# Optimization experiments

Measured on AMD Instinct MI355X. Metric: run time of the kernel, lower is better.

Reference implementation:

```python
import math
import jax, jax.numpy as jnp
import numpy as np

EPS = 1e-5
KS = 8          # emb_ks == emb_hs
NH = 4          # attention heads
LOOKBACK = 5
NLAYERS = 4


def prelu(x, a):
    return jnp.where(x >= 0, x, a * x)


def ln_c(x, g, b):
    # LayerNormalization4D: stats over channel dim; note (std + eps) denominator
    mu = jnp.mean(x, 1, keepdims=True)
    var = jnp.mean((x - mu) ** 2, 1, keepdims=True)
    return (x - mu) / (jnp.sqrt(var + EPS) + EPS) * g[None, :, None, None] + b[None, :, None, None]


def ln_cf_head(x, g, b):
    # x: [H, B, E, T, F]; stats over (E, F); g, b: [H, E, F]
    mu = jnp.mean(x, (2, 4), keepdims=True)
    var = jnp.mean((x - mu) ** 2, (2, 4), keepdims=True)
    return (x - mu) / (jnp.sqrt(var + EPS) + EPS) * g[:, None, :, None, :] + b[:, None, :, None, :]


def ln_cf_proj(x, g, b):
    # x: [B, C, T, F]; stats over (C, F); g, b: [C, F]
    mu = jnp.mean(x, (1, 3), keepdims=True)
    var = jnp.mean((x - mu) ** 2, (1, 3), keepdims=True)
    return (x - mu) / (jnp.sqrt(var + EPS) + EPS) * g[None, :, None, :] + b[None, :, None, :]


def lstm(x, wih, whh, bih, bhh):
    # x: [N, T, I] -> hidden sequence [N, T, H]; PyTorch gate order i, f, g, o
    xp = jnp.einsum('nti,gi->ntg', x, wih) + bih + bhh
    H = whh.shape[1]
    N = x.shape[0]

    def step(carry, xt):
        h, c = carry
        gates = xt + h @ whh.T
        i, f, g, o = jnp.split(gates, 4, axis=-1)
        c = jax.nn.sigmoid(f) * c + jax.nn.sigmoid(i) * jnp.tanh(g)
        h = jax.nn.sigmoid(o) * jnp.tanh(c)
        return (h, c), h

    init = (jnp.zeros((N, H), x.dtype), jnp.zeros((N, H), x.dtype))
    _, hs = jax.lax.scan(step, init, jnp.swapaxes(xp, 0, 1))
    return jnp.swapaxes(hs, 0, 1)


def bilstm(x, wih, whh, bih, bhh):
    fwd = lstm(x, wih[0], whh[0], bih[0], bhh[0])
    bwd = lstm(x[:, ::-1], wih[1], whh[1], bih[1], bhh[1])[:, ::-1]
    return jnp.concatenate([fwd, bwd], -1)


def unfold1d(x):
    # non-overlapping unfold (ks == stride == KS): [N, C, L] -> [N, L//KS, C*KS]
    N, C, Lx = x.shape
    return x.reshape(N, C, Lx // KS, KS).transpose(0, 2, 1, 3).reshape(N, Lx // KS, C * KS)


def fold1d(h, w, b):
    # ConvTranspose1d with stride == kernel == KS; h: [N, Lp, D], w: [D, C, KS]
    y = jnp.einsum('nld,dck->nlck', h, w)
    N, Lp, C, K = y.shape
    return y.transpose(0, 2, 1, 3).reshape(N, C, Lp * K) + b[None, :, None]


def conv2d(x, w, b):
    y = jax.lax.conv_general_dilated(x, w, (1, 1), ((1, 1), (1, 1)),
                                     dimension_numbers=('NCHW', 'OIHW', 'NCHW'))
    return y + b[None, :, None, None]


def block(x, p):
    B, C, oT, oF = x.shape
    T = math.ceil((oT - KS) / KS) * KS + KS
    F = math.ceil((oF - KS) / KS) * KS + KS
    x = jnp.pad(x, ((0, 0), (0, 0), (0, T - oT), (0, F - oF)))
    input_ = x
    # intra (frequency) bidirectional LSTM
    z = ln_c(input_, p['intra_norm_g'], p['intra_norm_b'])
    z = z.transpose(0, 2, 1, 3).reshape(B * T, C, F)
    z = unfold1d(z)                                    # [B*T, F//KS, C*KS]
    h = bilstm(z, p['intra_wih'], p['intra_whh'], p['intra_bih'], p['intra_bhh'])
    z = fold1d(h, p['intra_lin_w'], p['intra_lin_b'])  # [B*T, C, F]
    intra = z.reshape(B, T, C, F).transpose(0, 2, 1, 3) + input_
    # inter (time) causal LSTM
    z = ln_c(intra, p['inter_norm_g'], p['inter_norm_b'])
    z = z.transpose(0, 3, 1, 2).reshape(B * F, C, T)
    z = unfold1d(z)                                    # [B*F, T//KS, C*KS]
    h = lstm(z, p['inter_wih'], p['inter_whh'], p['inter_bih'], p['inter_bhh'])
    z = fold1d(h, p['inter_lin_w'], p['inter_lin_b'])  # [B*F, C, T]
    inter = z.reshape(B, F, C, T).transpose(0, 2, 3, 1) + intra
    inter = inter[..., :oT, :oF]

    # per-head 1x1-conv QKV (batched over heads) + local causal attention
    def qkv(w, b, a, g, beta):
        y = jnp.einsum('bctf,hec->hbetf', inter, w) + b[:, None, :, None, None]
        y = prelu(y, a[:, None, None, None, None])
        return ln_cf_head(y, g, beta)

    Q = qkv(p['q_w'], p['q_b'], p['q_a'], p['q_g'], p['q_beta'])
    K = qkv(p['k_w'], p['k_b'], p['k_a'], p['k_g'], p['k_beta'])
    V = qkv(p['v_w'], p['v_b'], p['v_a'], p['v_g'], p['v_beta'])
    E = Q.shape[2]
    CV = V.shape[2]
    Qf = Q.transpose(0, 1, 3, 2, 4).reshape(NH, B, oT, E * oF)
    Kf = K.transpose(0, 1, 3, 2, 4).reshape(NH, B, oT, E * oF)
    Vf = V.transpose(0, 1, 3, 2, 4).reshape(NH, B, oT, CV * oF)
    attn = jnp.einsum('hbtd,hbsd->hbts', Qf, Kf) / jnp.sqrt(jnp.asarray(E * oF, Qf.dtype))
    t = jnp.arange(oT)
    d = t[:, None] - t[None, :]
    mask = (d >= 0) & (d <= LOOKBACK)      # causal with 5-frame lookback
    attn = jnp.where(mask, attn, -1e30)
    A = jax.nn.softmax(attn, axis=-1)
    O = jnp.einsum('hbts,hbsd->hbtd', A, Vf).reshape(NH, B, oT, CV, oF)
    O = O.transpose(1, 0, 3, 2, 4).reshape(B, NH * CV, oT, oF)
    y = jnp.einsum('bctf,dc->bdtf', O, p['proj_w']) + p['proj_b'][None, :, None, None]
    y = prelu(y, p['proj_a'])
    y = ln_cf_proj(y, p['proj_g'], p['proj_beta'])
    return y + inter


def _forward(x, conv_w, conv_b, gn_g, gn_b,
             intra_norm_g, intra_norm_b, intra_wih, intra_whh, intra_bih, intra_bhh,
             intra_lin_w, intra_lin_b,
             inter_norm_g, inter_norm_b, inter_wih, inter_whh, inter_bih, inter_bhh,
             inter_lin_w, inter_lin_b,
             q_w, q_b, q_a, q_g, q_beta,
             k_w, k_b, k_a, k_g, k_beta,
             v_w, v_b, v_a, v_g, v_beta,
             proj_w, proj_b, proj_a, proj_g, proj_beta,
             deconv_w, deconv_b):
    esti = conv2d(x, conv_w, conv_b)
    # GroupNorm(1, emb_dim): per-sample stats over (C, T, F), per-channel affine
    mu = jnp.mean(esti, (1, 2, 3), keepdims=True)
    var = jnp.mean((esti - mu) ** 2, (1, 2, 3), keepdims=True)
    esti = (esti - mu) / jnp.sqrt(var + EPS) * gn_g[None, :, None, None] + gn_b[None, :, None, None]
    stacked = dict(
        intra_norm_g=intra_norm_g, intra_norm_b=intra_norm_b,
        intra_wih=intra_wih, intra_whh=intra_whh, intra_bih=intra_bih, intra_bhh=intra_bhh,
        intra_lin_w=intra_lin_w, intra_lin_b=intra_lin_b,
        inter_norm_g=inter_norm_g, inter_norm_b=inter_norm_b,
        inter_wih=inter_wih, inter_whh=inter_whh, inter_bih=inter_bih, inter_bhh=inter_bhh,
        inter_lin_w=inter_lin_w, inter_lin_b=inter_lin_b,
        q_w=q_w, q_b=q_b, q_a=q_a, q_g=q_g, q_beta=q_beta,
        k_w=k_w, k_b=k_b, k_a=k_a, k_g=k_g, k_beta=k_beta,
        v_w=v_w, v_b=v_b, v_a=v_a, v_g=v_g, v_beta=v_beta,
        proj_w=proj_w, proj_b=proj_b, proj_a=proj_a, proj_g=proj_g, proj_beta=proj_beta,
    )
    for l in range(NLAYERS):
        p = {k: v[l] for k, v in stacked.items()}
        esti = block(esti, p)
    # ConvTranspose2d(k=3, s=1, p=1) == conv with spatially flipped, io-swapped kernel, pad 1
    w2 = jnp.flip(deconv_w, (2, 3)).transpose(1, 0, 2, 3)
    return conv2d(esti, w2, deconv_b)


def setup_inputs() -> dict:
    key = jax.random.key(0)
    keys = iter(jax.random.split(key, 80))

    def rn(shape, s=0.05):
        return jax.random.normal(next(keys), shape, jnp.float32) * s

    L, C, H, E, CV, FA = 4, 32, 256, 4, 8, 161
    IN = C * KS
    return dict(
        x=jax.random.normal(next(keys), (8, 2, 504, 161), jnp.float32),
        conv_w=rn((C, 2, 3, 3)), conv_b=jnp.zeros((C,), jnp.float32),
        gn_g=jnp.ones((C,), jnp.float32), gn_b=jnp.zeros((C,), jnp.float32),
        intra_norm_g=jnp.ones((L, C), jnp.float32), intra_norm_b=jnp.zeros((L, C), jnp.float32),
        intra_wih=rn((L, 2, 4 * H, IN)), intra_whh=rn((L, 2, 4 * H, H)),
        intra_bih=jnp.zeros((L, 2, 4 * H), jnp.float32), intra_bhh=jnp.zeros((L, 2, 4 * H), jnp.float32),
        intra_lin_w=rn((L, 2 * H, C, KS)), intra_lin_b=jnp.zeros((L, C), jnp.float32),
        inter_norm_g=jnp.ones((L, C), jnp.float32), inter_norm_b=jnp.zeros((L, C), jnp.float32),
        inter_wih=rn((L, 4 * H, IN)), inter_whh=rn((L, 4 * H, H)),
        inter_bih=jnp.zeros((L, 4 * H), jnp.float32), inter_bhh=jnp.zeros((L, 4 * H), jnp.float32),
        inter_lin_w=rn((L, H, C, KS)), inter_lin_b=jnp.zeros((L, C), jnp.float32),
        q_w=rn((L, NH, E, C)), q_b=jnp.zeros((L, NH, E), jnp.float32),
        q_a=jnp.full((L, NH), 0.25, jnp.float32),
        q_g=jnp.ones((L, NH, E, FA), jnp.float32), q_beta=jnp.zeros((L, NH, E, FA), jnp.float32),
        k_w=rn((L, NH, E, C)), k_b=jnp.zeros((L, NH, E), jnp.float32),
        k_a=jnp.full((L, NH), 0.25, jnp.float32),
        k_g=jnp.ones((L, NH, E, FA), jnp.float32), k_beta=jnp.zeros((L, NH, E, FA), jnp.float32),
        v_w=rn((L, NH, CV, C)), v_b=jnp.zeros((L, NH, CV), jnp.float32),
        v_a=jnp.full((L, NH), 0.25, jnp.float32),
        v_g=jnp.ones((L, NH, CV, FA), jnp.float32), v_beta=jnp.zeros((L, NH, CV, FA), jnp.float32),
        proj_w=rn((L, C, C)), proj_b=jnp.zeros((L, C), jnp.float32),
        proj_a=jnp.full((L,), 0.25, jnp.float32),
        proj_g=jnp.ones((L, C, FA), jnp.float32), proj_beta=jnp.zeros((L, C, FA), jnp.float32),
        deconv_w=rn((C, 2, 3, 3)), deconv_b=jnp.zeros((2,), jnp.float32),
    )


def reference(x, conv_w, conv_b, gn_g, gn_b,
              intra_norm_g, intra_norm_b, intra_wih, intra_whh, intra_bih, intra_bhh,
              intra_lin_w, intra_lin_b,
              inter_norm_g, inter_norm_b, inter_wih, inter_whh, inter_bih, inter_bhh,
              inter_lin_w, inter_lin_b,
              q_w, q_b, q_a, q_g, q_beta,
              k_w, k_b, k_a, k_g, k_beta,
              v_w, v_b, v_a, v_g, v_beta,
              proj_w, proj_b, proj_a, proj_g, proj_beta,
              deconv_w, deconv_b):
    return _forward(x, conv_w, conv_b, gn_g, gn_b,
                    intra_norm_g, intra_norm_b, intra_wih, intra_whh, intra_bih, intra_bhh,
                    intra_lin_w, intra_lin_b,
                    inter_norm_g, inter_norm_b, inter_wih, inter_whh, inter_bih, inter_bhh,
                    inter_lin_w, inter_lin_b,
                    q_w, q_b, q_a, q_g, q_beta,
                    k_w, k_b, k_a, k_g, k_beta,
                    v_w, v_b, v_a, v_g, v_beta,
                    proj_w, proj_b, proj_a, proj_g, proj_beta,
                    deconv_w, deconv_b)
```

## Files before the change

kernel.cpp:

```cpp
#include <hip/hip_runtime.h>
#include <hip/hip_bf16.h>
#include <math.h>

#define BB   8
#define CH   32
#define TT   504
#define FFp  168
#define OF   161
#define KSZ  8
#define HID  256
#define NG   1024
#define NHh  4
#define EE   4
#define CVv  8
#define N1   4032
#define N2   1344
#define LFi  21
#define LTi  63
#define EPSf 1e-5f

#define AS1 __attribute__((address_space(1)))
#define AS3 __attribute__((address_space(3)))

typedef __hip_bfloat16 bf16;
typedef __attribute__((ext_vector_type(8))) short s16x8;
typedef __attribute__((ext_vector_type(4))) float f32x4;

__device__ __forceinline__ float b2f(bf16 v) { return __bfloat162float(v); }
__device__ __forceinline__ bf16 f2b(float v) { return __float2bfloat16(v); }
__device__ __forceinline__ float us2f(unsigned short u) {
  return __uint_as_float(((unsigned)u) << 16);
}
__device__ __forceinline__ unsigned short f2bu(float v) {
  unsigned u = __float_as_uint(v);
  unsigned r = u + 0x7fffu + ((u >> 16) & 1u);
  return (unsigned short)(r >> 16);
}

__device__ __forceinline__ float sigm(float x) { return 1.f / (1.f + __expf(-x)); }
__device__ __forceinline__ float tanh_f(float x) {
  x = fminf(15.f, fmaxf(-15.f, x));
  float e = __expf(2.f * x);
  return (e - 1.f) / (e + 1.f);
}

__device__ __forceinline__ void block_reduce2(float& s1, float& s2, float* red) {
#pragma unroll
  for (int off = 32; off > 0; off >>= 1) {
    s1 += __shfl_down(s1, off, 64);
    s2 += __shfl_down(s2, off, 64);
  }
  int lane = threadIdx.x & 63, wv = threadIdx.x >> 6;
  __syncthreads();
  if (lane == 0) { red[wv * 2] = s1; red[wv * 2 + 1] = s2; }
  __syncthreads();
  s1 = red[0] + red[2] + red[4] + red[6];
  s2 = red[1] + red[3] + red[5] + red[7];
}

__global__ __launch_bounds__(192) void conv_in_k(const float* __restrict__ x,
                                                 const float* __restrict__ w,
                                                 const float* __restrict__ bias,
                                                 bf16* __restrict__ out) {
  __shared__ float xs[2 * 3 * (OF + 3)];
  int bt = blockIdx.x;
  int b = bt / TT, t = bt % TT;
  int tid = threadIdx.x;
  for (int i = tid; i < 2 * 3 * (OF + 3); i += 192) {
    int ci = i / (3 * (OF + 3));
    int rem = i % (3 * (OF + 3));
    int rr = rem / (OF + 3);
    int f = rem % (OF + 3);
    int ts = t + rr - 1;
    float v = 0.f;
    if (ts >= 0 && ts < TT && f < OF) v = x[((size_t)(b * 2 + ci) * TT + ts) * OF + f];
    xs[i] = v;
  }
  __syncthreads();
  int f = tid;
  if (f < OF) {
    float xv[2][3][3];
#pragma unroll
    for (int ci = 0; ci < 2; ci++)
#pragma unroll
      for (int kh = 0; kh < 3; kh++)
#pragma unroll
        for (int kw = 0; kw < 3; kw++) {
          int ff = f + kw - 1;
          xv[ci][kh][kw] = (ff < 0) ? 0.f : xs[(ci * 3 + kh) * (OF + 3) + ff];
        }
    for (int co = 0; co < CH; co++) {
      float acc = bias[co];
#pragma unroll
      for (int ci = 0; ci < 2; ci++)
#pragma unroll
        for (int kh = 0; kh < 3; kh++)
#pragma unroll
          for (int kw = 0; kw < 3; kw++)
            acc += xv[ci][kh][kw] * w[((co * 2 + ci) * 3 + kh) * 3 + kw];
      out[((size_t)(b * CH + co) * TT + t) * OF + f] = f2b(acc);
    }
  }
}

__global__ __launch_bounds__(256) void gn_reduce_k(const bf16* __restrict__ xin,
                                                   float* __restrict__ stats) {
  const int M = CH * TT * OF;
  int b = blockIdx.x >> 6;
  int part = blockIdx.x & 63;
  const bf16* p = xin + (size_t)b * M;
  float s1 = 0.f, s2 = 0.f;
  for (int i = part * 256 + threadIdx.x; i < M; i += 64 * 256) {
    float v = b2f(p[i]);
    s1 += v; s2 += v * v;
  }
  __shared__ float red[8];
  block_reduce2(s1, s2, red);
  if (threadIdx.x == 0) {
    atomicAdd(&stats[b * 2], s1);
    atomicAdd(&stats[b * 2 + 1], s2);
  }
}

__global__ __launch_bounds__(256) void gn_apply_k(const bf16* __restrict__ xin,
                                                  const float* __restrict__ stats,
                                                  const float* __restrict__ g,
                                                  const float* __restrict__ bb,
                                                  bf16* __restrict__ act) {
  int gid = blockIdx.x * 256 + threadIdx.x;
  int f = gid % FFp;
  int t = (gid / FFp) % TT;
  int c = (gid / (FFp * TT)) % CH;
  int b = gid / (FFp * TT * CH);
  float v = 0.f;
  if (f < OF) {
    const float M = (float)(CH * TT * OF);
    float mu = stats[b * 2] / M;
    float var = stats[b * 2 + 1] / M - mu * mu;
    float xv = b2f(xin[((size_t)(b * CH + c) * TT + t) * OF + f]);
    v = (xv - mu) * rsqrtf(var + EPSf) * g[c] + bb[c];
  }
  act[gid] = f2b(v);
}

__global__ __launch_bounds__(256) void ln_unfold_k(const bf16* __restrict__ xin,
                                                   const float* __restrict__ g,
                                                   const float* __restrict__ bb,
                                                   bf16* __restrict__ out) {
  __shared__ float sm[CH * FFp];
  __shared__ float mu_s[FFp], rs_s[FFp];
  __shared__ float gg[CH], bv[CH];
  int bt = blockIdx.x;
  int b = bt / TT, t = bt % TT;
  int tid = threadIdx.x;
  if (tid < CH) { gg[tid] = g[tid]; bv[tid] = bb[tid]; }
  const bf16* base = xin + ((size_t)b * CH * TT + t) * FFp;
  for (int idx = tid; idx < CH * FFp; idx += 256) {
    int c = idx / FFp, f = idx % FFp;
    sm[idx] = b2f(base[(size_t)c * TT * FFp + f]);
  }
  __syncthreads();
  if (tid < FFp) {
    int f = tid;
    float s1 = 0.f, s2 = 0.f;
#pragma unroll
    for (int c = 0; c < CH; c++) { float v = sm[c * FFp + f]; s1 += v; s2 += v * v; }
    float mu = s1 / CH;
    float var = s2 / CH - mu * mu;
    mu_s[f] = mu;
    rs_s[f] = 1.f / (sqrtf(var + EPSf) + EPSf);
  }
  __syncthreads();
  unsigned short* outu = (unsigned short*)out;
  for (int ch = tid; ch < LFi * CH; ch += 256) {
    int gI = ch >> 5, c = ch & 31;
    float gc = gg[c], bc = bv[c];
    unsigned short o8[8];
#pragma unroll
    for (int k = 0; k < 8; k++) {
      int f = gI * 8 + k;
      float v = (sm[c * FFp + f] - mu_s[f]) * rs_s[f] * gc + bc;
      o8[k] = f2bu(v);
    }
    *(uint4*)(outu + ((size_t)gI * N1 + bt) * 256 + c * 8) = *(uint4*)o8;
  }
}

__global__ __launch_bounds__(256) void ln_unfold8_k(const bf16* __restrict__ xin,
                                                    const float* __restrict__ g,
                                                    const float* __restrict__ bb,
                                                    bf16* __restrict__ out) {
  __shared__ short smb[8 * CH * FFp];
  __shared__ float mu_s[8 * FFp], rs_s[8 * FFp];
  __shared__ float gg[CH], bv[CH];
  int tg = blockIdx.x, b = blockIdx.y;
  int tid = threadIdx.x;
  if (tid < CH) { gg[tid] = g[tid]; bv[tid] = bb[tid]; }
  const short* src = (const short*)xin;
  for (int idx = tid; idx < 8 * CH * (FFp / 8); idx += 256) {
    int t8 = idx / (CH * 21);
    int rem = idx % (CH * 21);
    int c = rem / 21, fc = rem % 21;
    s16x8 v = *(const s16x8*)(src + ((size_t)(b * CH + c) * TT + tg * 8 + t8) * FFp + fc * 8);
    *(s16x8*)(&smb[(t8 * CH + c) * FFp + fc * 8]) = v;
  }
  __syncthreads();
  for (int p = tid; p < 8 * FFp; p += 256) {
    int t8 = p / FFp, f = p % FFp;
    float s1 = 0.f, s2 = 0.f;
#pragma unroll
    for (int c = 0; c < CH; c++) {
      float v = us2f((unsigned short)smb[(t8 * CH + c) * FFp + f]);
      s1 += v; s2 += v * v;
    }
    float mu = s1 / CH;
    float var = s2 / CH - mu * mu;
    mu_s[p] = mu;
    rs_s[p] = 1.f / (sqrtf(var + EPSf) + EPSf);
  }
  __syncthreads();
  unsigned short* outu = (unsigned short*)out;
  for (int ch = tid; ch < FFp * CH; ch += 256) {
    int f = ch >> 5, c = ch & 31;
    float gc = gg[c], bc = bv[c];
    unsigned short o8[8];
#pragma unroll
    for (int k = 0; k < 8; k++) {
      float v = us2f((unsigned short)smb[(k * CH + c) * FFp + f]);
      v = (v - mu_s[k * FFp + f]) * rs_s[k * FFp + f] * gc + bc;
      o8[k] = f2bu(v);
    }
    *(uint4*)(outu + ((size_t)tg * N2 + b * FFp + f) * 256 + c * 8) = *(uint4*)o8;
  }
}

__global__ __launch_bounds__(256) void lstm_prep_k(const float* __restrict__ wih0,
                                                   const float* __restrict__ whh0,
                                                   bf16* __restrict__ blob0) {
  int dir = blockIdx.y;
  const float* wih = wih0 + (size_t)dir * 262144;
  const float* whh = whh0 + (size_t)dir * 262144;
  unsigned short* blob = (unsigned short*)(blob0 + (size_t)dir * 524288);
  int gid = blockIdx.x * 256 + threadIdx.x;
  int lane = gid & 63;
  int ks = (gid >> 6) & 15;
  int nt = gid >> 10;
  int n = nt * 16 + (lane & 15);
  int kb = ks * 32 + (lane >> 4) * 8;
  unsigned short o8[8];
#pragma unroll
  for (int j = 0; j < 8; j++) {
    int k = kb + j;
    float v = (k < 256) ? wih[n * 256 + k] : whh[n * 256 + (k - 256)];
    o8[j] = f2bu(v);
  }
  *(uint4*)(blob + (size_t)gid * 8) = *(uint4*)o8;
}

__global__ __launch_bounds__(512) void lstm_mfma_k(const bf16* __restrict__ xz,
                                                   const bf16* __restrict__ blob0,
                                                   const float* __restrict__ bih0,
                                                   const float* __restrict__ bhh0,
                                                   bf16* __restrict__ hout,
                                                   int N, int Ls, int hstride, int bidir) {
  __shared__ __attribute__((aligned(16))) short afr[16 * 64 * 8];
  extern __shared__ __attribute__((aligned(16))) short bstage[];
  int tid = threadIdx.x;
  int w = tid >> 6, lane = tid & 63;
  int l15 = lane & 15, lq = lane >> 4;
  int dir = blockIdx.y;
  const short* blob = (const short*)(blob0 + (size_t)dir * 524288);
  const float* bih = bih0 + dir * NG;
  const float* bhh = bhh0 + dir * NG;
  int hoff = dir * 256;
  int n0 = blockIdx.x * 16;
  unsigned short* houtu = (unsigned short*)hout;
  const short* xzs = (const short*)xz;
  short* bst_w = bstage + w * 4096;

  float bias[4][2];
#pragma unroll
  for (int q = 0; q < 4; q++)
#pragma unroll
    for (int j = 0; j < 2; j++) {
      int n = q * 256 + (2 * w + j) * 16 + l15;
      bias[q][j] = bih[n] + bhh[n];
    }
  for (int i = tid; i < 8 * 64 * 8; i += 512) afr[8 * 64 * 8 + i] = 0;
  float cst[8];
#pragma unroll
  for (int i = 0; i < 8; i++) cst[i] = 0.f;

#define BQ_ISSUE(C)                                                              \
  {                                                                              \
    int c32_ = (C) >> 1, h2_ = (C) & 1;                                          \
    int a_ = c32_ >> 3, r_ = c32_ & 7;                                           \
    int nt_ = (r_ >> 1) * 16 + 2 * w + (r_ & 1);                                 \
    const short* gb_ = blob + (size_t)nt_ * 8192 + (a_ * 4 + h2_ * 2) * 512 + lane * 8; \
    short* lb_ = bst_w + ((C) & 3) * 1024;                                       \
    _Pragma("unroll")                                                            \
    for (int k_ = 0; k_ < 2; k_++)                                               \
      __builtin_amdgcn_global_load_lds((const AS1 void*)(gb_ + k_ * 512),        \
                                       (AS3 void*)(lb_ + k_ * 512), 16, 0, 0);   \
  }

  for (int st = 0; st < Ls; st++) {
    int t = (bidir && dir) ? (Ls - 1 - st) : st;
    {
      const short* gx = xzs + ((size_t)t * N + n0 + (lane & 15)) * 256 + (w * 4 + (lane >> 4)) * 8;
      __builtin_amdgcn_global_load_lds((const AS1 void*)gx, (AS3 void*)(afr + w * 512), 16, 0, 0);
    }
    BQ_ISSUE(0);
    BQ_ISSUE(1);
    BQ_ISSUE(2);
    __syncthreads();

    f32x4 acc[4][2];
#pragma unroll
    for (int q = 0; q < 4; q++)
#pragma unroll
      for (int j = 0; j < 2; j++)
        acc[q][j] = (f32x4){bias[q][j], bias[q][j], bias[q][j], bias[q][j]};

    s16x8 af[4];
#pragma unroll
    for (int C = 0; C < 64; C++) {
      int c32 = C >> 1, h2 = C & 1;
      int a = c32 >> 3, r = c32 & 7;
      int q = r >> 1, j = r & 1;
      if (r == 0 && h2 == 0) {
#pragma unroll
        for (int k = 0; k < 4; k++)
          af[k] = *(const s16x8*)(&afr[((a * 4 + k) * 64 + lane) * 8]);
      }
      __builtin_amdgcn_s_waitcnt(0x0F74);
      const short* lb = bst_w + (C & 3) * 1024;
#pragma unroll
      for (int k = 0; k < 2; k++) {
        s16x8 bf = *(const s16x8*)(lb + k * 512 + lane * 8);
        acc[q][j] = __builtin_amdgcn_mfma_f32_16x16x32_bf16(af[h2 * 2 + k], bf, acc[q][j], 0, 0, 0);
      }
      if (C < 61) BQ_ISSUE(C + 3);
    }
    __syncthreads();

#pragma unroll
    for (int j = 0; j < 2; j++) {
      int d = (2 * w + j) * 16 + l15;
      int slot = (8 + (d >> 5)) * 64 + ((d >> 3) & 3) * 16;
#pragma unroll
      for (int r = 0; r < 4; r++) {
        int m = lq * 4 + r;
        float iv = sigm(acc[0][j][r]);
        float fv = sigm(acc[1][j][r]);
        float gv = tanh_f(acc[2][j][r]);
        float ov = sigm(acc[3][j][r]);
        float c = fv * cst[j * 4 + r] + iv * gv;
        cst[j * 4 + r] = c;
        float h = ov * tanh_f(c);
        unsigned short hb = f2bu(h);
        houtu[((size_t)t * N + n0 + m) * hstride + hoff + d] = hb;
        afr[(slot + m) * 8 + (d & 7)] = (short)hb;
      }
    }
  }
#undef BQ_ISSUE
}

__global__ __launch_bounds__(256) void fold_gemm_k(const bf16* __restrict__ A,
                                                   const float* __restrict__ Bw,
                                                   const float* __restrict__ linb,
                                                   const bf16* __restrict__ resid,
                                                   bf16* __restrict__ outp,
                                                   int K, int mode) {
  __shared__ float As[16 * 68];
  __shared__ float Bs[16 * 64];
  int tid = threadIdx.x;
  int n0 = blockIdx.x * 64;
  int m0 = blockIdx.y * 64;
  int tr = tid >> 4, tc = tid & 15;
  float acc[4][4] = {};
  int arow = tid >> 2, akg = (tid & 3) * 4;
  int bkk = tid >> 4, bc4 = (tid & 15) * 4;
  for (int k0 = 0; k0 < K; k0 += 16) {
    ushort4 avu = *(const ushort4*)((const unsigned short*)A + (size_t)(m0 + arow) * K + k0 + akg);
    float4 bv = *(const float4*)(Bw + (size_t)(k0 + bkk) * 256 + n0 + bc4);
    __syncthreads();
    As[(akg + 0) * 68 + arow] = us2f(avu.x);
    As[(akg + 1) * 68 + arow] = us2f(avu.y);
    As[(akg + 2) * 68 + arow] = us2f(avu.z);
    As[(akg + 3) * 68 + arow] = us2f(avu.w);
    *(float4*)(&Bs[bkk * 64 + bc4]) = bv;
    __syncthreads();
#pragma unroll
    for (int kk = 0; kk < 16; kk++) {
      float4 a4 = *(const float4*)(&As[kk * 68 + tr * 4]);
      float4 b4 = *(const float4*)(&Bs[kk * 64 + tc * 4]);
      float aa[4] = {a4.x, a4.y, a4.z, a4.w};
      float bb_[4] = {b4.x, b4.y, b4.z, b4.w};
#pragma unroll
      for (int i = 0; i < 4; i++)
#pragma unroll
        for (int j = 0; j < 4; j++) acc[i][j] += aa[i] * bb_[j];
    }
  }
#pragma unroll
  for (int i = 0; i < 4; i++) {
    int r = m0 + tr * 4 + i;
#pragma unroll
    for (int j = 0; j < 4; j++) {
      int col = n0 + tc * 4 + j;
      int c = col >> 3, kp = col & 7;
      float v = acc[i][j] + linb[c];
      if (mode == 0) {
        int l = r / N1, n = r % N1;
        int b = n / TT, t = n % TT;
        size_t o = ((size_t)(b * CH + c) * TT + t) * FFp + (l * 8 + kp);
        outp[o] = f2b(v + b2f(resid[o]));
      } else {
        int l = r / N2, n = r % N2;
        int b = n / FFp, fq = n % FFp;
        int t = l * 8 + kp;
        if (fq < OF) {
          size_t o = ((size_t)(b * CH + c) * TT + t) * OF + fq;
          size_t ri = ((size_t)(b * CH + c) * TT + t) * FFp + fq;
          outp[o] = f2b(v + b2f(resid[ri]));
        }
      }
    }
  }
}

__global__ __launch_bounds__(256) void qkv_k(const bf16* __restrict__ interc,
    const float* __restrict__ qw, const float* __restrict__ qb, const float* __restrict__ qa,
    const float* __restrict__ qg, const float* __restrict__ qbeta,
    const float* __restrict__ kw, const float* __restrict__ kb, const float* __restrict__ ka,
    const float* __restrict__ kg, const float* __restrict__ kbeta,
    const float* __restrict__ vw, const float* __restrict__ vb, const float* __restrict__ va,
    const float* __restrict__ vg, const float* __restrict__ vbeta,
    bf16* __restrict__ qo, bf16* __restrict__ ko, bf16* __restrict__ vo) {
  __shared__ float sm[CH * OF];
  __shared__ float wb[16 * 32];
  __shared__ float wbias[16];
  __shared__ float yb[16 * OF];
  __shared__ float red[8];
  int bt = blockIdx.x, h = blockIdx.y;
  int b = bt / TT, t = bt % TT;
  int tid = threadIdx.x;
  const bf16* src = interc + ((size_t)b * CH * TT + t) * OF;
  for (int idx = tid; idx < CH * OF; idx += 256) {
    int c = idx / OF, f = idx % OF;
    sm[idx] = b2f(src[(size_t)c * TT * OF + f]);
  }
  for (int idx = tid; idx < 512; idx += 256) {
    int e = idx >> 5, c = idx & 31;
    float w;
    if (e < 4) w = qw[(h * 4 + e) * 32 + c];
    else if (e < 8) w = kw[(h * 4 + e - 4) * 32 + c];
    else w = vw[(h * 8 + e - 8) * 32 + c];
    wb[idx] = w;
  }
  if (tid < 16) {
    float bv;
    if (tid < 4) bv = qb[h * 4 + tid];
    else if (tid < 8) bv = kb[h * 4 + tid - 4];
    else bv = vb[h * 8 + tid - 8];
    wbias[tid] = bv;
  }
  __syncthreads();
  float aQ = qa[h], aK = ka[h], aV = va[h];
  for (int idx = tid; idx < 16 * OF; idx += 256) {
    int e = idx / OF, f = idx % OF;
    float accv = wbias[e];
#pragma unroll
    for (int c = 0; c < 32; c++) accv += sm[c * OF + f] * wb[e * 32 + c];
    float a = e < 4 ? aQ : (e < 8 ? aK : aV);
    yb[idx] = accv >= 0.f ? accv : a * accv;
  }
  __syncthreads();
  for (int seg = 0; seg < 3; seg++) {
    int s0 = (seg == 0) ? 0 : ((seg == 1) ? 644 : 1288);
    int len = (seg == 2) ? 1288 : 644;
    float s1 = 0.f, s2 = 0.f;
    for (int i = tid; i < len; i += 256) { float v = yb[s0 + i]; s1 += v; s2 += v * v; }
    block_reduce2(s1, s2, red);
    float mu = s1 / len;
    float var = s2 / len - mu * mu;
    float rs = 1.f / (sqrtf(var + EPSf) + EPSf);
    const float* gp; const float* bp; bf16* op; int nch;
    if (seg == 0) { gp = qg; bp = qbeta; op = qo; nch = 4; }
    else if (seg == 1) { gp = kg; bp = kbeta; op = ko; nch = 4; }
    else { gp = vg; bp = vbeta; op = vo; nch = 8; }
    for (int i = tid; i < len; i += 256) {
      int e = i / OF, f = i % OF;
      float v = (yb[s0 + i] - mu) * rs * gp[(h * nch + e) * OF + f] + bp[(h * nch + e) * OF + f];
      op[(((size_t)(h * BB + b) * nch + e) * TT + t) * OF + f] = f2b(v);
    }
  }
}

__global__ __launch_bounds__(256) void attn_k(const bf16* __restrict__ Q,
                                              const bf16* __restrict__ Kt,
                                              const bf16* __restrict__ V,
                                              bf16* __restrict__ O) {
  int t = blockIdx.x;
  int hb = blockIdx.y;
  int h = hb >> 3, b = hb & 7;
  int tid = threadIdx.x;
  int nv = min(t, 5) + 1;
  const float scale = 0.0394055201f;
  __shared__ float redl[24];
  float part[6] = {0, 0, 0, 0, 0, 0};
  size_t qkbase = ((size_t)(h * BB + b) * EE) * TT * OF;
  for (int i = tid; i < EE * OF; i += 256) {
    int e = i / OF, f = i % OF;
    float qv = b2f(Q[qkbase + ((size_t)e * TT + t) * OF + f]);
#pragma unroll
    for (int d = 0; d < 6; d++)
      if (d < nv) part[d] += qv * b2f(Kt[qkbase + ((size_t)e * TT + (t - d)) * OF + f]);
  }
#pragma unroll
  for (int d = 0; d < 6; d++)
#pragma unroll
    for (int off = 32; off > 0; off >>= 1) part[d] += __shfl_down(part[d], off, 64);
  int lane = tid & 63, wv = tid >> 6;
  if (lane == 0) {
#pragma unroll
    for (int d = 0; d < 6; d++) redl[wv * 6 + d] = part[d];
  }
  __syncthreads();
  float a[6], sv[6];
  float m = -1e30f;
#pragma unroll
  for (int d = 0; d < 6; d++)
    if (d < nv) {
      float s = (redl[d] + redl[6 + d] + redl[12 + d] + redl[18 + d]) * scale;
      sv[d] = s;
      m = fmaxf(m, s);
    }
  float denom = 0.f;
#pragma unroll
  for (int d = 0; d < 6; d++)
    if (d < nv) { a[d] = __expf(sv[d] - m); denom += a[d]; }
  float inv = 1.f / denom;
  size_t vbase = ((size_t)(h * BB + b) * CVv) * TT * OF;
  for (int i = tid; i < CVv * OF; i += 256) {
    int cv = i / OF, f = i % OF;
    float o = 0.f;
#pragma unroll
    for (int d = 0; d < 6; d++)
      if (d < nv) o += a[d] * b2f(V[vbase + ((size_t)cv * TT + (t - d)) * OF + f]);
    O[(((size_t)b * CH + h * CVv + cv) * TT + t) * OF + f] = f2b(o * inv);
  }
}

__global__ __launch_bounds__(256) void proj_k(const bf16* __restrict__ ob,
                                              const float* __restrict__ pw,
                                              const float* __restrict__ pb,
                                              const float* __restrict__ pa,
                                              const float* __restrict__ pg,
                                              const float* __restrict__ pbeta,
                                              const bf16* __restrict__ interc,
                                              bf16* __restrict__ act) {
  __shared__ float sm[CH * OF];
  __shared__ float wsm[CH * CH];
  __shared__ float yb[CH * OF];
  __shared__ float red[8];
  int bt = blockIdx.x;
  int b = bt / TT, t = bt % TT;
  int tid = threadIdx.x;
  const bf16* src = ob + ((size_t)b * CH * TT + t) * OF;
  for (int idx = tid; idx < CH * OF; idx += 256) {
    int c = idx / OF, f = idx % OF;
    sm[idx] = b2f(src[(size_t)c * TT * OF + f]);
  }
  for (int idx = tid; idx < CH * CH; idx += 256) wsm[idx] = pw[idx];
  __syncthreads();
  float aP = pa[0];
  for (int idx = tid; idx < CH * OF; idx += 256) {
    int d = idx / OF, f = idx % OF;
    float accv = pb[d];
#pragma unroll
    for (int c = 0; c < 32; c++) accv += sm[c * OF + f] * wsm[d * 32 + c];
    yb[idx] = accv >= 0.f ? accv : aP * accv;
  }
  __syncthreads();
  float s1 = 0.f, s2 = 0.f;
  for (int i = tid; i < CH * OF; i += 256) { float v = yb[i]; s1 += v; s2 += v * v; }
  block_reduce2(s1, s2, red);
  const float Mn = (float)(CH * OF);
  float mu = s1 / Mn;
  float var = s2 / Mn - mu * mu;
  float rs = 1.f / (sqrtf(var + EPSf) + EPSf);
  for (int idx = tid; idx < CH * FFp; idx += 256) {
    int d = idx / FFp, f = idx % FFp;
    float v = 0.f;
    if (f < OF) {
      float y = (yb[d * OF + f] - mu) * rs * pg[d * OF + f] + pbeta[d * OF + f];
      v = y + b2f(interc[((size_t)(b * CH + d) * TT + t) * OF + f]);
    }
    act[((size_t)(b * CH + d) * TT + t) * FFp + f] = f2b(v);
  }
}

__global__ __launch_bounds__(256) void deconv_k(const bf16* __restrict__ act,
                                                const float* __restrict__ w,
                                                const float* __restrict__ bias,
                                                float* __restrict__ out) {
  __shared__ float ash[CH * 3 * FFp];
  int bt = blockIdx.x;
  int b = bt / TT, t = bt % TT;
  int tid = threadIdx.x;
  const short* acts = (const short*)act;
  for (int ch = tid; ch < CH * 3 * (FFp / 8); ch += 256) {
    int ci = ch / 63, rem = ch % 63;
    int rr = rem / 21, fc = rem % 21;
    int ts = t + rr - 1;
    float* dst = &ash[(ci * 3 + rr) * FFp + fc * 8];
    if (ts < 0 || ts >= TT) {
#pragma unroll
      for (int k2 = 0; k2 < 8; k2++) dst[k2] = 0.f;
    } else {
      s16x8 v = *(const s16x8*)(acts + ((size_t)(b * CH + ci) * TT + ts) * FFp + fc * 8);
#pragma unroll
      for (int k2 = 0; k2 < 8; k2++) dst[k2] = us2f((unsigned short)v[k2]);
    }
  }
  __syncthreads();
  int f = tid;
  if (f < OF) {
    float acc0 = bias[0], acc1 = bias[1];
#pragma unroll 4
    for (int ci = 0; ci < CH; ci++) {
      const float* row = &ash[ci * 3 * FFp];
      float xv[3][3];
#pragma unroll
      for (int kh = 0; kh < 3; kh++)
#pragma unroll
        for (int kw = 0; kw < 3; kw++) {
          int ff = f + kw - 1;
          xv[kh][kw] = (ff < 0) ? 0.f : row[kh * FFp + ff];
        }
#pragma unroll
      for (int kh = 0; kh < 3; kh++)
#pragma unroll
        for (int kw = 0; kw < 3; kw++) {
          acc0 += xv[kh][kw] * w[((ci * 2 + 0) * 3 + (2 - kh)) * 3 + (2 - kw)];
          acc1 += xv[kh][kw] * w[((ci * 2 + 1) * 3 + (2 - kh)) * 3 + (2 - kw)];
        }
    }
    out[((size_t)(b * 2 + 0) * TT + t) * OF + f] = acc0;
    out[((size_t)(b * 2 + 1) * TT + t) * OF + f] = acc1;
  }
}

extern "C" void kernel_launch(void* const* d_in, const int* in_sizes, int n_in,
                              void* d_out, int out_size, void* d_ws, size_t ws_size,
                              hipStream_t stream) {
  const float* x            = (const float*)d_in[0];
  const float* conv_w       = (const float*)d_in[1];
  const float* conv_b       = (const float*)d_in[2];
  const float* gn_g         = (const float*)d_in[3];
  const float* gn_b         = (const float*)d_in[4];
  const float* intra_norm_g = (const float*)d_in[5];
  const float* intra_norm_b = (const float*)d_in[6];
  const float* intra_wih    = (const float*)d_in[7];
  const float* intra_whh    = (const float*)d_in[8];
  const float* intra_bih    = (const float*)d_in[9];
  const float* intra_bhh    = (const float*)d_in[10];
  const float* intra_lin_w  = (const float*)d_in[11];
  const float* intra_lin_b  = (const float*)d_in[12];
  const float* inter_norm_g = (const float*)d_in[13];
  const float* inter_norm_b = (const float*)d_in[14];
  const float* inter_wih    = (const float*)d_in[15];
  const float* inter_whh    = (const float*)d_in[16];
  const float* inter_bih    = (const float*)d_in[17];
  const float* inter_bhh    = (const float*)d_in[18];
  const float* inter_lin_w  = (const float*)d_in[19];
  const float* inter_lin_b  = (const float*)d_in[20];
  const float* q_w    = (const float*)d_in[21];
  const float* q_b    = (const float*)d_in[22];
  const float* q_a    = (const float*)d_in[23];
  const float* q_g    = (const float*)d_in[24];
  const float* q_beta = (const float*)d_in[25];
  const float* k_w    = (const float*)d_in[26];
  const float* k_b    = (const float*)d_in[27];
  const float* k_a    = (const float*)d_in[28];
  const float* k_g    = (const float*)d_in[29];
  const float* k_beta = (const float*)d_in[30];
  const float* v_w    = (const float*)d_in[31];
  const float* v_b    = (const float*)d_in[32];
  const float* v_a    = (const float*)d_in[33];
  const float* v_g    = (const float*)d_in[34];
  const float* v_beta = (const float*)d_in[35];
  const float* proj_w    = (const float*)d_in[36];
  const float* proj_b    = (const float*)d_in[37];
  const float* proj_a    = (const float*)d_in[38];
  const float* proj_g    = (const float*)d_in[39];
  const float* proj_beta = (const float*)d_in[40];
  const float* deconv_w  = (const float*)d_in[41];
  const float* deconv_b  = (const float*)d_in[42];

  float* stats = (float*)d_ws;
  bf16* arena  = (bf16*)((char*)d_ws + 256);
  bf16* act    = arena;
  bf16* tmp    = arena + 21676032;
  bf16* hbuf   = arena + 43352064;
  bf16* res    = arena + 86704128;
  bf16* interc = arena + 108380160;
  bf16* convout = interc;
  bf16* qbuf = act;
  bf16* kbuf = tmp;
  bf16* vbuf = res;
  bf16* obuf = hbuf;
  bf16* blob_intra = res;
  bf16* blob_inter = interc;

  hipMemsetAsync(stats, 0, 64 * sizeof(float), stream);
  conv_in_k<<<4032, 192, 0, stream>>>(x, conv_w, conv_b, convout);
  gn_reduce_k<<<512, 256, 0, stream>>>(convout, stats);
  gn_apply_k<<<84672, 256, 0, stream>>>(convout, stats, gn_g, gn_b, act);

  for (int l = 0; l < 4; l++) {
    lstm_prep_k<<<dim3(256, 2), 256, 0, stream>>>(
        intra_wih + (size_t)l * 524288, intra_whh + (size_t)l * 524288, blob_intra);
    ln_unfold_k<<<4032, 256, 0, stream>>>(act, intra_norm_g + l * 32, intra_norm_b + l * 32, tmp);
    lstm_mfma_k<<<dim3(252, 2), 512, 65536, stream>>>(
        tmp, blob_intra, intra_bih + l * 2048, intra_bhh + l * 2048, hbuf, N1, LFi, 512, 1);
    fold_gemm_k<<<dim3(4, 1323), 256, 0, stream>>>(
        hbuf, intra_lin_w + (size_t)l * 131072, intra_lin_b + l * 32, act, res, 512, 0);
    lstm_prep_k<<<dim3(256, 1), 256, 0, stream>>>(
        inter_wih + (size_t)l * 262144, inter_whh + (size_t)l * 262144, blob_inter);
    ln_unfold8_k<<<dim3(LTi, BB), 256, 0, stream>>>(res, inter_norm_g + l * 32, inter_norm_b + l * 32, tmp);
    lstm_mfma_k<<<dim3(84, 1), 512, 65536, stream>>>(
        tmp, blob_inter, inter_bih + l * 1024, inter_bhh + l * 1024, hbuf, N2, LTi, 256, 0);
    fold_gemm_k<<<dim3(4, 1323), 256, 0, stream>>>(
        hbuf, inter_lin_w + (size_t)l * 65536, inter_lin_b + l * 32, res, interc, 256, 1);
    qkv_k<<<dim3(4032, 4), 256, 0, stream>>>(interc,
        q_w + l * 512, q_b + l * 16, q_a + l * 4, q_g + l * 2576, q_beta + l * 2576,
        k_w + l * 512, k_b + l * 16, k_a + l * 4, k_g + l * 2576, k_beta + l * 2576,
        v_w + l * 1024, v_b + l * 32, v_a + l * 4, v_g + l * 5152, v_beta + l * 5152,
        qbuf, kbuf, vbuf);
    attn_k<<<dim3(504, 32), 256, 0, stream>>>(qbuf, kbuf, vbuf, obuf);
    proj_k<<<4032, 256, 0, stream>>>(obuf, proj_w + l * 1024, proj_b + l * 32, proj_a + l,
                                     proj_g + l * 5152, proj_beta + l * 5152, interc, act);
  }
  deconv_k<<<4032, 256, 0, stream>>>(act, deconv_w, deconv_b, (float*)d_out);
}
```

Measured before the change: 16.39 ms.

## Process two 16-row M tiles per LSTM block to reuse streamed weights

Each LSTM block now handles 32 sequences instead of 16. Every weight fragment streamed into LDS now feeds two MFMAs, one per M tile, which halves total weight traffic and halves the grid size. The cost is more registers for accumulators and cell state, a larger LDS activation buffer, and fewer blocks. The intra LSTM grid drops to 252 blocks and the inter grid to 42 blocks, which may leave CUs idle on a 256-CU part. The waitcnt values at the end of the loop were adjusted to match the changed count of outstanding loads.

Result: faster. 15.92 ms (-2.8%).

```diff
diff --git a/kernel.cpp b/kernel.cpp
--- a/kernel.cpp
+++ b/kernel.cpp
@@ -263,7 +263,7 @@
                                                    const float* __restrict__ bhh0,
                                                    bf16* __restrict__ hout,
                                                    int N, int Ls, int hstride, int bidir) {
-  __shared__ __attribute__((aligned(16))) short afr[16 * 64 * 8];
+  __shared__ __attribute__((aligned(16))) short afr[16 * 2 * 64 * 8];
   extern __shared__ __attribute__((aligned(16))) short bstage[];
   int tid = threadIdx.x;
   int w = tid >> 6, lane = tid & 63;
@@ -273,7 +273,7 @@
   const float* bih = bih0 + dir * NG;
   const float* bhh = bhh0 + dir * NG;
   int hoff = dir * 256;
-  int n0 = blockIdx.x * 16;
+  int n0 = blockIdx.x * 32;
   unsigned short* houtu = (unsigned short*)hout;
   const short* xzs = (const short*)xz;
   short* bst_w = bstage + w * 4096;
@@ -286,10 +286,10 @@
       int n = q * 256 + (2 * w + j) * 16 + l15;
       bias[q][j] = bih[n] + bhh[n];
     }
-  for (int i = tid; i < 8 * 64 * 8; i += 512) afr[8 * 64 * 8 + i] = 0;
-  float cst[8];
-#pragma unroll
-  for (int i = 0; i < 8; i++) cst[i] = 0.f;
+  for (int i = tid; i < 8192; i += 512) afr[8192 + i] = 0;
+  float cst[16];
+#pragma unroll
+  for (int i = 0; i < 16; i++) cst[i] = 0.f;
 
 #define BQ_ISSUE(C)                                                              \
   {                                                                              \
@@ -307,62 +307,75 @@
   for (int st = 0; st < Ls; st++) {
     int t = (bidir && dir) ? (Ls - 1 - st) : st;
     {
-      const short* gx = xzs + ((size_t)t * N + n0 + (lane & 15)) * 256 + (w * 4 + (lane >> 4)) * 8;
-      __builtin_amdgcn_global_load_lds((const AS1 void*)gx, (AS3 void*)(afr + w * 512), 16, 0, 0);
+      const short* gx = xzs + ((size_t)t * N + n0 + l15) * 256 + (w * 4 + lq) * 8;
+      __builtin_amdgcn_global_load_lds((const AS1 void*)gx,
+                                       (AS3 void*)(afr + (w * 2 + 0) * 512), 16, 0, 0);
+      __builtin_amdgcn_global_load_lds((const AS1 void*)(gx + 16 * 256),
+                                       (AS3 void*)(afr + (w * 2 + 1) * 512), 16, 0, 0);
     }
     BQ_ISSUE(0);
     BQ_ISSUE(1);
     BQ_ISSUE(2);
     __syncthreads();
 
-    f32x4 acc[4][2];
-#pragma unroll
-    for (int q = 0; q < 4; q++)
-#pragma unroll
-      for (int j = 0; j < 2; j++)
-        acc[q][j] = (f32x4){bias[q][j], bias[q][j], bias[q][j], bias[q][j]};
-
-    s16x8 af[4];
+    f32x4 acc[2][4][2];
+#pragma unroll
+    for (int mt = 0; mt < 2; mt++)
+#pragma unroll
+      for (int q = 0; q < 4; q++)
+#pragma unroll
+        for (int j = 0; j < 2; j++)
+          acc[mt][q][j] = (f32x4){bias[q][j], bias[q][j], bias[q][j], bias[q][j]};
+
+    s16x8 af[4][2];
 #pragma unroll
     for (int C = 0; C < 64; C++) {
       int c32 = C >> 1, h2 = C & 1;
-      int a = c32 >> 3, r = c32 & 7;
-      int q = r >> 1, j = r & 1;
-      if (r == 0 && h2 == 0) {
+      int rR = c32 & 7;
+      int q = rR >> 1, j = rR & 1;
+      if (rR == 0 && h2 == 0) {
+        int a = c32 >> 3;
 #pragma unroll
         for (int k = 0; k < 4; k++)
-          af[k] = *(const s16x8*)(&afr[((a * 4 + k) * 64 + lane) * 8]);
+#pragma unroll
+          for (int mt = 0; mt < 2; mt++)
+            af[k][mt] = *(const s16x8*)(&afr[(((a * 4 + k) * 2 + mt) * 64 + lane) * 8]);
       }
-      __builtin_amdgcn_s_waitcnt(0x0F74);
+      if (C < 62)       __builtin_amdgcn_s_waitcnt(0x0F74);
+      else if (C == 62) __builtin_amdgcn_s_waitcnt(0x0F72);
+      else              __builtin_amdgcn_s_waitcnt(0x0F70);
       const short* lb = bst_w + (C & 3) * 1024;
 #pragma unroll
       for (int k = 0; k < 2; k++) {
         s16x8 bf = *(const s16x8*)(lb + k * 512 + lane * 8);
-        acc[q][j] = __builtin_amdgcn_mfma_f32_16x16x32_bf16(af[h2 * 2 + k], bf, acc[q][j], 0, 0, 0);
+        acc[0][q][j] = __builtin_amdgcn_mfma_f32_16x16x32_bf16(af[h2 * 2 + k][0], bf, acc[0][q][j], 0, 0, 0);
+        acc[1][q][j] = __builtin_amdgcn_mfma_f32_16x16x32_bf16(af[h2 * 2 + k][1], bf, acc[1][q][j], 0, 0, 0);
       }
       if (C < 61) BQ_ISSUE(C + 3);
     }
     __syncthreads();
 
 #pragma unroll
-    for (int j = 0; j < 2; j++) {
-      int d = (2 * w + j) * 16 + l15;
-      int slot = (8 + (d >> 5)) * 64 + ((d >> 3) & 3) * 16;
-#pragma unroll
-      for (int r = 0; r < 4; r++) {
-        int m = lq * 4 + r;
-        float iv = sigm(acc[0][j][r]);
-        float fv = sigm(acc[1][j][r]);
-        float gv = tanh_f(acc[2][j][r]);
-        float ov = sigm(acc[3][j][r]);
-        float c = fv * cst[j * 4 + r] + iv * gv;
-        cst[j * 4 + r] = c;
-        float h = ov * tanh_f(c);
-        unsigned short hb = f2bu(h);
-        houtu[((size_t)t * N + n0 + m) * hstride + hoff + d] = hb;
-        afr[(slot + m) * 8 + (d & 7)] = (short)hb;
+    for (int mt = 0; mt < 2; mt++)
+#pragma unroll
+      for (int j = 0; j < 2; j++) {
+        int d = (2 * w + j) * 16 + l15;
+        int slotb = ((8 + (d >> 5)) * 2 + mt) * 64 + ((d >> 3) & 3) * 16;
+#pragma unroll
+        for (int r = 0; r < 4; r++) {
+          int m = lq * 4 + r;
+          float iv = sigm(acc[mt][0][j][r]);
+          float fv = sigm(acc[mt][1][j][r]);
+          float gv = tanh_f(acc[mt][2][j][r]);
+          float ov = sigm(acc[mt][3][j][r]);
+          float c = fv * cst[mt * 8 + j * 4 + r] + iv * gv;
+          cst[mt * 8 + j * 4 + r] = c;
+          float h = ov * tanh_f(c);
+          unsigned short hb = f2bu(h);
+          houtu[((size_t)t * N + n0 + mt * 16 + m) * hstride + hoff + d] = hb;
+          afr[(slotb + m) * 8 + (d & 7)] = (short)hb;
+        }
       }
-    }
   }
 #undef BQ_ISSUE
 }
@@ -725,14 +738,14 @@
     lstm_prep_k<<<dim3(256, 2), 256, 0, stream>>>(
         intra_wih + (size_t)l * 524288, intra_whh + (size_t)l * 524288, blob_intra);
     ln_unfold_k<<<4032, 256, 0, stream>>>(act, intra_norm_g + l * 32, intra_norm_b + l * 32, tmp);
-    lstm_mfma_k<<<dim3(252, 2), 512, 65536, stream>>>(
+    lstm_mfma_k<<<dim3(126, 2), 512, 65536, stream>>>(
         tmp, blob_intra, intra_bih + l * 2048, intra_bhh + l * 2048, hbuf, N1, LFi, 512, 1);
     fold_gemm_k<<<dim3(4, 1323), 256, 0, stream>>>(
         hbuf, intra_lin_w + (size_t)l * 131072, intra_lin_b + l * 32, act, res, 512, 0);
     lstm_prep_k<<<dim3(256, 1), 256, 0, stream>>>(
         inter_wih + (size_t)l * 262144, inter_whh + (size_t)l * 262144, blob_inter);
     ln_unfold8_k<<<dim3(LTi, BB), 256, 0, stream>>>(res, inter_norm_g + l * 32, inter_norm_b + l * 32, tmp);
-    lstm_mfma_k<<<dim3(84, 1), 512, 65536, stream>>>(
+    lstm_mfma_k<<<dim3(42, 1), 512, 65536, stream>>>(
         tmp, blob_inter, inter_bih + l * 1024, inter_bhh + l * 1024, hbuf, N2, LTi, 256, 0);
     fold_gemm_k<<<dim3(4, 1323), 256, 0, stream>>>(
         hbuf, inter_lin_w + (size_t)l * 65536, inter_lin_b + l * 32, res, interc, 256, 1);
```
